# Optimization experiments

Hardware: AMD Instinct MI355X
Metric: run time of the kernel (lower is better)

The kernel has to match this reference:

```python
import jax, jax.numpy as jnp
import numpy as np

D_MODEL = 1024
N_HEAD = 16
D_K = 64
D_V = 64
D_INNER = 4096
MAX_REL = 16
EPS = 1e-6


def _rel_index(length_q, length_k):
    # Shaw-style clipped relative distance matrix -> indices into embedding table
    dist = jnp.arange(length_k)[None, :] - jnp.arange(length_q)[:, None]
    return jnp.clip(dist, -MAX_REL, MAX_REL) + MAX_REL  # [Lq, Lk] in [0, 2*MAX_REL]


def _layer_norm(x, gamma, beta):
    mu = jnp.mean(x, axis=-1, keepdims=True)
    var = jnp.var(x, axis=-1, keepdims=True)
    return (x - mu) / jnp.sqrt(var + EPS) * gamma + beta


def setup_inputs() -> dict:
    key = jax.random.key(0)
    ks = jax.random.split(key, 16)
    B, L = 8, 1024
    s = 0.02
    inp = {
        "q": jax.random.normal(ks[0], (B, L, D_MODEL), jnp.float32),
        "k": jax.random.normal(ks[1], (B, L, D_MODEL), jnp.float32),
        "v": jax.random.normal(ks[2], (B, L, D_MODEL), jnp.float32),
        "wq": jax.random.normal(ks[3], (D_MODEL, D_MODEL), jnp.float32) * s,
        "bq": jnp.zeros((D_MODEL,), jnp.float32),
        "wk": jax.random.normal(ks[4], (D_MODEL, D_MODEL), jnp.float32) * s,
        "bk": jnp.zeros((D_MODEL,), jnp.float32),
        "wv": jax.random.normal(ks[5], (D_MODEL, D_MODEL), jnp.float32) * s,
        "bv": jnp.zeros((D_MODEL,), jnp.float32),
        "wfc": jax.random.normal(ks[6], (D_MODEL, D_MODEL), jnp.float32) * s,
        "bfc": jnp.zeros((D_MODEL,), jnp.float32),
        "w1": jax.random.normal(ks[7], (D_MODEL, D_INNER), jnp.float32) * s,
        "b1": jnp.zeros((D_INNER,), jnp.float32),
        "w2": jax.random.normal(ks[8], (D_INNER, D_MODEL), jnp.float32) * s,
        "b2": jnp.zeros((D_MODEL,), jnp.float32),
        "ln_g": jnp.ones((D_MODEL,), jnp.float32),
        "ln_b": jnp.zeros((D_MODEL,), jnp.float32),
        "rel_k": jax.random.normal(ks[9], (2 * MAX_REL + 1, D_K), jnp.float32) * s,
        "rel_v": jax.random.normal(ks[10], (2 * MAX_REL + 1, D_V), jnp.float32) * s,
    }
    return inp


def reference(q, k, v, wq, bq, wk, bk, wv, bv, wfc, bfc, w1, b1, w2, b2, ln_g, ln_b, rel_k, rel_v):
    B, Lq, _ = q.shape
    Lk = k.shape[1]
    residual = q

    Q = q @ wq + bq  # [B, Lq, D]
    K = k @ wk + bk
    V = v @ wv + bv

    Qh = Q.reshape(B, Lq, N_HEAD, D_K)  # [B, Lq, H, dk]
    Kh = K.reshape(B, Lk, N_HEAD, D_K)
    Vh = V.reshape(B, Lk, N_HEAD, D_V)

    # content-content scores
    attn1 = jnp.einsum("bqhd,bkhd->bhqk", Qh, Kh)
    # content-position scores (Shaw relative position)
    idx = _rel_index(Lq, Lk)  # [Lq, Lk]
    k2 = rel_k[idx]           # [Lq, Lk, dk]
    attn2 = jnp.einsum("bqhd,qkd->bhqk", Qh, k2)

    attn = (attn1 + attn2) / jnp.sqrt(jnp.float32(D_K))
    attn = jax.nn.softmax(attn, axis=-1)  # dropout = identity (eval)

    weight1 = jnp.einsum("bhqk,bkhd->bhqd", attn, Vh)
    v2 = rel_v[idx]  # [Lq, Lk, dv]
    weight2 = jnp.einsum("bhqk,qkd->bhqd", attn, v2)

    out = (weight1 + weight2).transpose(0, 2, 1, 3).reshape(B, Lq, N_HEAD * D_V)
    out = out @ wfc + bfc
    out = out + residual
    out = _layer_norm(out, ln_g, ln_b)

    residual = out
    out2 = jax.nn.relu(out @ w1 + b1) @ w2 + b2
    out = _layer_norm(out2 + residual, ln_g, ln_b)  # same LN params reused, as in source
    return out
```

## Files before the change

### kernel.cpp

```cpp
#include <hip/hip_runtime.h>
#include <stdint.h>


typedef __bf16 bf16x8 __attribute__((ext_vector_type(8)));
typedef float  f32x4  __attribute__((ext_vector_type(4)));

__device__ __forceinline__ unsigned short f2bf(float f) {
  __bf16 h = (__bf16)f;
  union { __bf16 h; unsigned short u; } x; x.h = h;
  return x.u;
}
__device__ __forceinline__ float bf2f(unsigned short h) {
  union { unsigned u; float f; } x; x.u = ((unsigned)h) << 16; return x.f;
}

__device__ __forceinline__ void gload_lds16(
    const unsigned short* g,
    __attribute__((address_space(3))) unsigned int* l) {
  __builtin_amdgcn_global_load_lds(
      (const __attribute__((address_space(1))) unsigned int*)g, l, 16, 0, 0);
}

template<int EPI>
__global__ __launch_bounds__(256, 4) void gemm_bt(
    const unsigned short* __restrict__ A,
    const unsigned short* __restrict__ Bt,
    const float* __restrict__ bias0,
    const float* __restrict__ bias1,
    const float* __restrict__ bias2,
    void* __restrict__ Cout,
    int M, int N, int K,
    size_t sA, size_t sB, size_t sC)
{
  __shared__ __align__(16) unsigned short As[2][128 * 32];
  __shared__ __align__(16) unsigned short Bs[2][128 * 32];
  const int tid = threadIdx.x;
  const int lane = tid & 63, wv = tid >> 6;
  const int lq = lane >> 4, lm = lane & 15;
  const int wr = wv >> 1, wc = wv & 1;

  const int z = blockIdx.z;
  const float* bias = (z == 0) ? bias0 : (z == 1) ? bias1 : bias2;
  A  += (size_t)z * sA;
  Bt += (size_t)z * sB;

  const int nx = gridDim.x;
  const int nwg = nx * gridDim.y;
  int bid = blockIdx.y * nx + blockIdx.x;
  bid = (bid & 7) * (nwg >> 3) + (bid >> 3);
  const int m0 = (bid / nx) * 128, n0 = (bid % nx) * 128;

  const unsigned short* ga0 = A  + (size_t)(m0 + (tid >> 2)) * K + (tid & 3) * 8;
  const unsigned short* gb0 = Bt + (size_t)(n0 + (tid >> 2)) * K + (tid & 3) * 8;
  const size_t rstep = (size_t)64 * K;

  __attribute__((address_space(3))) unsigned int* lA =
      (__attribute__((address_space(3))) unsigned int*)As + wv * 256;
  __attribute__((address_space(3))) unsigned int* lB =
      (__attribute__((address_space(3))) unsigned int*)Bs + wv * 256;

  const char* fa = (const char*)As + (wr * 64 + lm) * 64 + lq * 16;
  const char* fb = (const char*)Bs + (wc * 64 + lm) * 64 + lq * 16;

  f32x4 acc[4][4] = {};

  auto compute_tile = [&](int b) {
    bf16x8 af[4], bfr[4];
    #pragma unroll
    for (int i = 0; i < 4; ++i) af[i]  = *(const bf16x8*)(fa + b * 8192 + i * 1024);
    #pragma unroll
    for (int j = 0; j < 4; ++j) bfr[j] = *(const bf16x8*)(fb + b * 8192 + j * 1024);
    #pragma unroll
    for (int i = 0; i < 4; ++i)
      #pragma unroll
      for (int j = 0; j < 4; ++j)
        acc[i][j] = __builtin_amdgcn_mfma_f32_16x16x32_bf16(af[i], bfr[j], acc[i][j], 0, 0, 0);
  };

  const int nk = K >> 5;
  gload_lds16(ga0,         lA);
  gload_lds16(ga0 + rstep, lA + 1024);
  gload_lds16(gb0,         lB);
  gload_lds16(gb0 + rstep, lB + 1024);
  ga0 += 32; gb0 += 32;
  __syncthreads();

  int cur = 0;
  for (int kt = 0; kt < nk - 1; ++kt) {
    const int nb = cur ^ 1;
    gload_lds16(ga0,         lA + nb * 2048);
    gload_lds16(ga0 + rstep, lA + nb * 2048 + 1024);
    gload_lds16(gb0,         lB + nb * 2048);
    gload_lds16(gb0 + rstep, lB + nb * 2048 + 1024);
    ga0 += 32; gb0 += 32;
    compute_tile(cur);
    __syncthreads();
    cur = nb;
  }
  compute_tile(cur);

  #pragma unroll
  for (int i = 0; i < 4; ++i) {
    #pragma unroll
    for (int j = 0; j < 4; ++j) {
      const int col = n0 + wc * 64 + j * 16 + lm;
      const float bv = bias[col];
      #pragma unroll
      for (int r = 0; r < 4; ++r) {
        const int row = m0 + wr * 64 + i * 16 + lq * 4 + r;
        float v = acc[i][j][r] + bv;
        if (EPI == 2) v = fmaxf(v, 0.0f);
        if (EPI == 1) ((float*)Cout)[(size_t)row * N + col] = v;
        else ((unsigned short*)Cout + (size_t)z * sC)[(size_t)row * N + col] = f2bf(v);
      }
    }
  }
}

__global__ __launch_bounds__(256) void tcast(
    const float* __restrict__ in, unsigned short* __restrict__ out, int R, int C)
{
  __shared__ float tile[32][33];
  const int tx = threadIdx.x & 31, ty = threadIdx.x >> 5;
  const int r0 = blockIdx.y * 32, c0 = blockIdx.x * 32;
  #pragma unroll
  for (int s = 0; s < 4; ++s)
    tile[ty + s * 8][tx] = in[(size_t)(r0 + ty + s * 8) * C + c0 + tx];
  __syncthreads();
  #pragma unroll
  for (int s = 0; s < 4; ++s)
    out[(size_t)(c0 + ty + s * 8) * R + r0 + tx] = f2bf(tile[tx][ty + s * 8]);
}

__global__ __launch_bounds__(256) void cast4(
    const float* __restrict__ in, unsigned short* __restrict__ out, int n)
{
  int i = (blockIdx.x * 256 + threadIdx.x) * 4;
  if (i < n) {
    float4 v = *(const float4*)(in + i);
    ushort4 o;
    o.x = f2bf(v.x); o.y = f2bf(v.y); o.z = f2bf(v.z); o.w = f2bf(v.w);
    *(ushort4*)(out + i) = o;
  }
}

__global__ __launch_bounds__(256) void vtrans(
    const unsigned short* __restrict__ VP, unsigned short* __restrict__ VPT)
{
  __shared__ unsigned short tile[64 * 66];
  const int pt = blockIdx.x, h = blockIdx.y, b = blockIdx.z;
  const int tid = threadIdx.x;
  const int p = tid >> 2, c0 = (tid & 3) * 16;
  const unsigned short* src = VP + (size_t)(b * 1024 + pt * 64 + p) * 1024 + h * 64 + c0;
  union { uint4 q; unsigned int u[4]; } t0, t1;
  t0.q = *(const uint4*)src;
  t1.q = *(const uint4*)(src + 8);
  #pragma unroll
  for (int e = 0; e < 4; ++e) {
    *(unsigned int*)&tile[p * 66 + c0 + e * 2]     = t0.u[e];
    *(unsigned int*)&tile[p * 66 + c0 + 8 + e * 2] = t1.u[e];
  }
  __syncthreads();
  const int d = tid >> 2, p0 = (tid & 3) * 16;
  union { uint4 q[2]; unsigned short s[16]; } ob;
  #pragma unroll
  for (int e = 0; e < 16; ++e) ob.s[e] = tile[(p0 + e) * 66 + d];
  unsigned short* dst = VPT + ((size_t)(h * 64 + d) * 8 + b) * 1024 + pt * 64 + p0;
  *(uint4*)dst       = ob.q[0];
  *(uint4*)(dst + 8) = ob.q[1];
}

__global__ __launch_bounds__(256, 3) void attn_flash(
    const unsigned short* __restrict__ Qp,
    const unsigned short* __restrict__ Kp,
    const unsigned short* __restrict__ VPT,
    const float* __restrict__ relk,
    const float* __restrict__ relv,
    unsigned short* __restrict__ ctx)
{
  int id = (blockIdx.z * gridDim.y + blockIdx.y) * gridDim.x + blockIdx.x;
  id = (id & 7) * 256 + (id >> 3);
  const int qt = id & 15, h = (id >> 4) & 15, b = id >> 8;

  const int tid = threadIdx.x;
  const int lane = tid & 63, wv = tid >> 6;
  const int lq = lane >> 4, lm = lane & 15;

  __shared__ __align__(16) unsigned short Kt[64][72];
  __shared__ __align__(16) unsigned short Vt[64][72];
  __shared__ __align__(16) unsigned short Pt[64][72];
  __shared__ __align__(16) unsigned short relvT[64][32];
  __shared__ float qrel_s[64][33];
  __shared__ float Racc[64][33];

  const float CE = 0.125f * 1.44269504088896340736f;

  const int tok0 = b * 1024 + qt * 64;

  for (int i = tid; i < 64 * 33; i += 256) {
    const int rr = i / 33, ss = i - rr * 33;
    Racc[rr][ss] = 0.0f;
  }
  for (int i = tid; i < 64 * 32; i += 256) {
    const int dd = i >> 5, ss = i & 31;
    relvT[dd][ss] = f2bf(relv[ss * 64 + dd]);
  }

  bf16x8 qf0, qf1;
  {
    const unsigned short* qg = Qp + (size_t)(tok0 + wv * 16 + lm) * 1024 + h * 64;
    qf0 = *(const bf16x8*)(qg + lq * 8);
    qf1 = *(const bf16x8*)(qg + 32 + lq * 8);
  }

  #pragma unroll
  for (int t = 0; t < 3; ++t) {
    const int bin = t * 16 + lm;
    union { bf16x8 v; unsigned short s[8]; } rk0, rk1;
    #pragma unroll
    for (int e = 0; e < 8; ++e) { rk0.s[e] = 0; rk1.s[e] = 0; }
    if (bin < 33) {
      const float* rp = relk + bin * 64 + lq * 8;
      #pragma unroll
      for (int e = 0; e < 8; ++e) {
        rk0.s[e] = f2bf(rp[e]);
        rk1.s[e] = f2bf(rp[32 + e]);
      }
    }
    f32x4 Sr = {};
    Sr = __builtin_amdgcn_mfma_f32_16x16x32_bf16(qf0, rk0.v, Sr, 0, 0, 0);
    Sr = __builtin_amdgcn_mfma_f32_16x16x32_bf16(qf1, rk1.v, Sr, 0, 0, 0);
    if (bin < 33) {
      #pragma unroll
      for (int r = 0; r < 4; ++r) qrel_s[wv * 16 + lq * 4 + r][bin] = Sr[r] * CE;
    }
  }
  __syncthreads();

  float q0a[4], q32a[4];
  #pragma unroll
  for (int r = 0; r < 4; ++r) {
    const int rowl = wv * 16 + lq * 4 + r;
    q0a[r]  = qrel_s[rowl][0];
    q32a[r] = qrel_s[rowl][32];
  }

  union { bf16x8 v; unsigned short s[8]; } one8;
  #pragma unroll
  for (int e = 0; e < 8; ++e) one8.s[e] = 0x3F80;

  f32x4 Oa[4] = {};
  f32x4 Rs = {};
  float r0a[4] = {0, 0, 0, 0}, r32a[4] = {0, 0, 0, 0};

  const int srow = tid >> 2, scol = (tid & 3) * 16;
  const unsigned short* kg = Kp + (size_t)(b * 1024 + srow) * 1024 + h * 64 + scol;
  const unsigned short* vg = VPT + ((size_t)(h * 64 + srow) * 8 + b) * 1024 + scol;
  const int qa0 = qt * 64 + wv * 16;

  const int pread = wv * 16 + ((lm & 3) << 2) + (lm >> 2);

  uint4 rk0_ = *(const uint4*)(kg);
  uint4 rk1_ = *(const uint4*)(kg + 8);
  uint4 rv0_ = *(const uint4*)(vg);
  uint4 rv1_ = *(const uint4*)(vg + 8);

  for (int kt = 0; kt < 16; ++kt) {
    __syncthreads();
    *(uint4*)&Kt[srow][scol]     = rk0_;
    *(uint4*)&Kt[srow][scol + 8] = rk1_;
    *(uint4*)&Vt[srow][scol]     = rv0_;
    *(uint4*)&Vt[srow][scol + 8] = rv1_;
    if (kt < 15) {
      kg += 64 * 1024;
      vg += 64;
      rk0_ = *(const uint4*)(kg);
      rk1_ = *(const uint4*)(kg + 8);
      rv0_ = *(const uint4*)(vg);
      rv1_ = *(const uint4*)(vg + 8);
    }
    __syncthreads();

    #pragma unroll
    for (int tj = 0; tj < 4; ++tj) {
      bf16x8 kf0 = *(const bf16x8*)(&Kt[tj * 16 + lm][lq * 8]);
      bf16x8 kf1 = *(const bf16x8*)(&Kt[tj * 16 + lm][32 + lq * 8]);
      f32x4 S = {};
      S = __builtin_amdgcn_mfma_f32_16x16x32_bf16(qf0, kf0, S, 0, 0, 0);
      S = __builtin_amdgcn_mfma_f32_16x16x32_bf16(qf1, kf1, S, 0, 0, 0);
      const int c0 = kt * 64 + tj * 16;
      const int prow0 = wv * 16 + lq;
      if (c0 + 31 <= qa0) {
        #pragma unroll
        for (int r = 0; r < 4; ++r) {
          const float p = __builtin_amdgcn_exp2f(fmaf(S[r], CE, q0a[r]));
          r0a[r] += p;
          Pt[prow0 + r * 4][tj * 16 + lm] = f2bf(p);
        }
      } else if (c0 >= qa0 + 31) {
        #pragma unroll
        for (int r = 0; r < 4; ++r) {
          const float p = __builtin_amdgcn_exp2f(fmaf(S[r], CE, q32a[r]));
          r32a[r] += p;
          Pt[prow0 + r * 4][tj * 16 + lm] = f2bf(p);
        }
      } else {
        const int kpos = c0 + lm;
        #pragma unroll
        for (int r = 0; r < 4; ++r) {
          const int rowl = wv * 16 + lq * 4 + r;
          const int dist = kpos - (qt * 64 + rowl);
          const int bin = (dist < -16 ? 0 : (dist > 16 ? 32 : dist + 16));
          const float p = __builtin_amdgcn_exp2f(fmaf(S[r], CE, qrel_s[rowl][bin]));
          if (bin == 0)       r0a[r]  += p;
          else if (bin == 32) r32a[r] += p;
          else Racc[rowl][bin] = p;
          Pt[prow0 + r * 4][tj * 16 + lm] = f2bf(p);
        }
      }
    }
    __syncthreads();
    bf16x8 pf0 = *(const bf16x8*)(&Pt[pread][lq * 8]);
    bf16x8 pf1 = *(const bf16x8*)(&Pt[pread][32 + lq * 8]);
    Rs = __builtin_amdgcn_mfma_f32_16x16x32_bf16(pf0, one8.v, Rs, 0, 0, 0);
    Rs = __builtin_amdgcn_mfma_f32_16x16x32_bf16(pf1, one8.v, Rs, 0, 0, 0);
    #pragma unroll
    for (int dt = 0; dt < 4; ++dt) {
      bf16x8 vf0 = *(const bf16x8*)(&Vt[dt * 16 + lm][lq * 8]);
      bf16x8 vf1 = *(const bf16x8*)(&Vt[dt * 16 + lm][32 + lq * 8]);
      Oa[dt] = __builtin_amdgcn_mfma_f32_16x16x32_bf16(pf0, vf0, Oa[dt], 0, 0, 0);
      Oa[dt] = __builtin_amdgcn_mfma_f32_16x16x32_bf16(pf1, vf1, Oa[dt], 0, 0, 0);
    }
  }

  #pragma unroll
  for (int r = 0; r < 4; ++r) {
    #pragma unroll
    for (int off = 1; off < 16; off <<= 1) {
      r0a[r]  += __shfl_xor(r0a[r],  off, 64);
      r32a[r] += __shfl_xor(r32a[r], off, 64);
    }
  }
  if (lm == 0) {
    #pragma unroll
    for (int r = 0; r < 4; ++r) Racc[wv * 16 + lq * 4 + r][0] = r0a[r];
  }
  __syncthreads();
  for (int i = tid; i < 64 * 32; i += 256) {
    const int rr = i >> 5, cc = i & 31;
    Pt[rr][cc] = f2bf(Racc[rr][cc]);
  }
  __syncthreads();

  bf16x8 raf = *(const bf16x8*)(&Pt[wv * 16 + lm][lq * 8]);
  #pragma unroll
  for (int dt = 0; dt < 4; ++dt) {
    bf16x8 rvb = *(const bf16x8*)(&relvT[dt * 16 + lm][lq * 8]);
    f32x4 O2 = {};
    O2 = __builtin_amdgcn_mfma_f32_16x16x32_bf16(raf, rvb, O2, 0, 0, 0);
    const float rv32 = relv[32 * 64 + dt * 16 + lm];
    #pragma unroll
    for (int r = 0; r < 4; ++r) {
      const int rowl = wv * 16 + lq * 4 + r;
      const float v = (Oa[dt][r] + O2[r] + r32a[r] * rv32) / Rs[r];
      ctx[(size_t)(tok0 + rowl) * 1024 + h * 64 + dt * 16 + lm] = f2bf(v);
    }
  }
}

template<bool WB>
__global__ __launch_bounds__(256) void ln_res(
    const float* __restrict__ x, const float* __restrict__ res,
    const float* __restrict__ g, const float* __restrict__ bta,
    float* __restrict__ of, unsigned short* __restrict__ ob)
{
  const int row = blockIdx.x;
  const int tid = threadIdx.x;
  __shared__ float red[8];
  const size_t base = (size_t)row * 1024 + tid * 4;
  const float4 xv = *(const float4*)(x + base);
  const float4 rv = *(const float4*)(res + base);
  float v0 = xv.x + rv.x, v1 = xv.y + rv.y, v2 = xv.z + rv.z, v3 = xv.w + rv.w;
  float s1 = v0 + v1 + v2 + v3;
  float s2 = v0 * v0 + v1 * v1 + v2 * v2 + v3 * v3;
  #pragma unroll
  for (int off = 1; off < 64; off <<= 1) {
    s1 += __shfl_xor(s1, off, 64);
    s2 += __shfl_xor(s2, off, 64);
  }
  const int wv = tid >> 6;
  if ((tid & 63) == 0) { red[wv * 2] = s1; red[wv * 2 + 1] = s2; }
  __syncthreads();
  s1 = red[0] + red[2] + red[4] + red[6];
  s2 = red[1] + red[3] + red[5] + red[7];
  const float mean = s1 * (1.f / 1024.f);
  const float var = s2 * (1.f / 1024.f) - mean * mean;
  const float rstd = rsqrtf(var + 1e-6f);
  const float4 gv = *(const float4*)(g + tid * 4);
  const float4 bv = *(const float4*)(bta + tid * 4);
  float y0 = (v0 - mean) * rstd * gv.x + bv.x;
  float y1 = (v1 - mean) * rstd * gv.y + bv.y;
  float y2 = (v2 - mean) * rstd * gv.z + bv.z;
  float y3 = (v3 - mean) * rstd * gv.w + bv.w;
  float4 yo; yo.x = y0; yo.y = y1; yo.z = y2; yo.w = y3;
  *(float4*)(of + base) = yo;
  if (WB) {
    ushort4 o;
    o.x = f2bf(y0); o.y = f2bf(y1); o.z = f2bf(y2); o.w = f2bf(y3);
    *(ushort4*)(ob + base) = o;
  }
}

extern "C" void kernel_launch(void* const* d_in, const int* in_sizes, int n_in,
                              void* d_out, int out_size, void* d_ws, size_t ws_size,
                              hipStream_t stream) {
  (void)in_sizes; (void)n_in; (void)out_size; (void)ws_size;
  const float* q    = (const float*)d_in[0];
  const float* k    = (const float*)d_in[1];
  const float* v    = (const float*)d_in[2];
  const float* wq   = (const float*)d_in[3];
  const float* bq   = (const float*)d_in[4];
  const float* wk   = (const float*)d_in[5];
  const float* bk   = (const float*)d_in[6];
  const float* wv_  = (const float*)d_in[7];
  const float* bv   = (const float*)d_in[8];
  const float* wfc  = (const float*)d_in[9];
  const float* bfc  = (const float*)d_in[10];
  const float* w1   = (const float*)d_in[11];
  const float* b1   = (const float*)d_in[12];
  const float* w2   = (const float*)d_in[13];
  const float* b2   = (const float*)d_in[14];
  const float* ln_g = (const float*)d_in[15];
  const float* ln_b = (const float*)d_in[16];
  const float* rel_k = (const float*)d_in[17];
  const float* rel_v = (const float*)d_in[18];

  char* ws = (char*)d_ws;
  const size_t MB = 1ull << 20;
  unsigned short* WQT  = (unsigned short*)(ws + 0 * MB);
  unsigned short* WKT  = (unsigned short*)(ws + 2 * MB);
  unsigned short* WVT  = (unsigned short*)(ws + 4 * MB);
  unsigned short* WFCT = (unsigned short*)(ws + 6 * MB);
  unsigned short* W1T  = (unsigned short*)(ws + 8 * MB);
  unsigned short* W2T  = (unsigned short*)(ws + 16 * MB);
  unsigned short* QP   = (unsigned short*)(ws + 24 * MB);
  unsigned short* KP   = (unsigned short*)(ws + 40 * MB);
  unsigned short* VP   = (unsigned short*)(ws + 56 * MB);
  unsigned short* QBF  = (unsigned short*)(ws + 72 * MB);
  unsigned short* KBF  = (unsigned short*)(ws + 88 * MB);
  unsigned short* VBF  = (unsigned short*)(ws + 104 * MB);
  unsigned short* VPT  = QBF;
  unsigned short* CTX  = KBF;
  float*          OTMP = (float*)(ws + 104 * MB);
  float*          X1F  = (float*)(ws + 24 * MB);
  unsigned short* X1BF = VP;
  unsigned short* HBUF = (unsigned short*)(ws + 72 * MB);
  float*          Y2   = (float*)(ws + 136 * MB);

  const dim3 blk(256);
  const int NTOK = 8192;

  tcast<<<dim3(32, 32), blk, 0, stream>>>(wq, WQT, 1024, 1024);
  tcast<<<dim3(32, 32), blk, 0, stream>>>(wk, WKT, 1024, 1024);
  tcast<<<dim3(32, 32), blk, 0, stream>>>(wv_, WVT, 1024, 1024);
  tcast<<<dim3(32, 32), blk, 0, stream>>>(wfc, WFCT, 1024, 1024);
  tcast<<<dim3(128, 32), blk, 0, stream>>>(w1, W1T, 1024, 4096);
  tcast<<<dim3(32, 128), blk, 0, stream>>>(w2, W2T, 4096, 1024);
  cast4<<<8192, blk, 0, stream>>>(q, QBF, NTOK * 1024);
  cast4<<<8192, blk, 0, stream>>>(k, KBF, NTOK * 1024);
  cast4<<<8192, blk, 0, stream>>>(v, VBF, NTOK * 1024);

  gemm_bt<0><<<dim3(8, 64, 3), blk, 0, stream>>>(
      QBF, WQT, bq, bk, bv, QP, NTOK, 1024, 1024,
      (size_t)8 * MB, (size_t)1 * MB, (size_t)8 * MB);

  vtrans<<<dim3(16, 16, 8), blk, 0, stream>>>(VP, VPT);

  attn_flash<<<dim3(16, 16, 8), blk, 0, stream>>>(QP, KP, VPT, rel_k, rel_v, CTX);

  gemm_bt<1><<<dim3(8, 64), blk, 0, stream>>>(CTX, WFCT, bfc, bfc, bfc, OTMP,
                                              NTOK, 1024, 1024, 0, 0, 0);
  ln_res<true><<<8192, blk, 0, stream>>>(OTMP, q, ln_g, ln_b, X1F, X1BF);
  gemm_bt<2><<<dim3(32, 64), blk, 0, stream>>>(X1BF, W1T, b1, b1, b1, HBUF,
                                               NTOK, 4096, 1024, 0, 0, 0);
  gemm_bt<1><<<dim3(8, 64), blk, 0, stream>>>(HBUF, W2T, b2, b2, b2, Y2,
                                              NTOK, 1024, 4096, 0, 0, 0);
  ln_res<false><<<8192, blk, 0, stream>>>(Y2, X1F, ln_g, ln_b, (float*)d_out, nullptr);
}
```

Baseline: 610.9 us.

## Triple-buffer GEMM LDS pipeline and load attention K/V fragments directly from global

The GEMM moves from double to triple buffering with async global-to-LDS loads, explicit vmcnt waits and a single barrier per k-step, so loads stay two tiles ahead of compute. The attention kernel drops the K/V shared-memory staging and its barriers and reads MFMA fragments straight from global memory (L2/L1), with occupancy raised to 4. The attention change removes the P-tile barrier before Pt is read, and each wave only reads its own 16 rows of Pt, so that should still be safe. Direct global fragment loads may cost more latency and bandwidth than LDS reuse across the 4 waves, and the larger GEMM LDS footprint lowers its occupancy hint.

```diff
diff --git a/kernel.cpp b/kernel.cpp
--- a/kernel.cpp
+++ b/kernel.cpp
@@ -22,7 +22,7 @@
 }
 
 template<int EPI>
-__global__ __launch_bounds__(256, 4) void gemm_bt(
+__global__ __launch_bounds__(256, 3) void gemm_bt(
     const unsigned short* __restrict__ A,
     const unsigned short* __restrict__ Bt,
     const float* __restrict__ bias0,
@@ -32,8 +32,8 @@
     int M, int N, int K,
     size_t sA, size_t sB, size_t sC)
 {
-  __shared__ __align__(16) unsigned short As[2][128 * 32];
-  __shared__ __align__(16) unsigned short Bs[2][128 * 32];
+  __shared__ __align__(16) unsigned short As[3][128 * 32];
+  __shared__ __align__(16) unsigned short Bs[3][128 * 32];
   const int tid = threadIdx.x;
   const int lane = tid & 63, wv = tid >> 6;
   const int lq = lane >> 4, lm = lane & 15;
@@ -64,12 +64,19 @@
 
   f32x4 acc[4][4] = {};
 
-  auto compute_tile = [&](int b) {
+  auto stage = [&](int buf) {
+    gload_lds16(ga0,         lA + buf * 2048);
+    gload_lds16(ga0 + rstep, lA + buf * 2048 + 1024);
+    gload_lds16(gb0,         lB + buf * 2048);
+    gload_lds16(gb0 + rstep, lB + buf * 2048 + 1024);
+    ga0 += 32; gb0 += 32;
+  };
+  auto compute_tile = [&](int buf) {
     bf16x8 af[4], bfr[4];
     #pragma unroll
-    for (int i = 0; i < 4; ++i) af[i]  = *(const bf16x8*)(fa + b * 8192 + i * 1024);
-    #pragma unroll
-    for (int j = 0; j < 4; ++j) bfr[j] = *(const bf16x8*)(fb + b * 8192 + j * 1024);
+    for (int i = 0; i < 4; ++i) af[i]  = *(const bf16x8*)(fa + buf * 8192 + i * 1024);
+    #pragma unroll
+    for (int j = 0; j < 4; ++j) bfr[j] = *(const bf16x8*)(fb + buf * 8192 + j * 1024);
     #pragma unroll
     for (int i = 0; i < 4; ++i)
       #pragma unroll
@@ -78,26 +85,25 @@
   };
 
   const int nk = K >> 5;
-  gload_lds16(ga0,         lA);
-  gload_lds16(ga0 + rstep, lA + 1024);
-  gload_lds16(gb0,         lB);
-  gload_lds16(gb0 + rstep, lB + 1024);
-  ga0 += 32; gb0 += 32;
-  __syncthreads();
-
-  int cur = 0;
-  for (int kt = 0; kt < nk - 1; ++kt) {
-    const int nb = cur ^ 1;
-    gload_lds16(ga0,         lA + nb * 2048);
-    gload_lds16(ga0 + rstep, lA + nb * 2048 + 1024);
-    gload_lds16(gb0,         lB + nb * 2048);
-    gload_lds16(gb0 + rstep, lB + nb * 2048 + 1024);
-    ga0 += 32; gb0 += 32;
-    compute_tile(cur);
-    __syncthreads();
-    cur = nb;
-  }
-  compute_tile(cur);
+  stage(0);
+  stage(1);
+  int t = 0;
+  for (; t < nk - 2; ++t) {
+    asm volatile("s_waitcnt vmcnt(4)" ::: "memory");
+    __builtin_amdgcn_s_barrier();
+    __builtin_amdgcn_sched_barrier(0);
+    stage((t + 2) % 3);
+    compute_tile(t % 3);
+  }
+  asm volatile("s_waitcnt vmcnt(4)" ::: "memory");
+  __builtin_amdgcn_s_barrier();
+  __builtin_amdgcn_sched_barrier(0);
+  compute_tile(t % 3);
+  ++t;
+  asm volatile("s_waitcnt vmcnt(0)" ::: "memory");
+  __builtin_amdgcn_s_barrier();
+  __builtin_amdgcn_sched_barrier(0);
+  compute_tile(t % 3);
 
   #pragma unroll
   for (int i = 0; i < 4; ++i) {
@@ -170,7 +176,7 @@
   *(uint4*)(dst + 8) = ob.q[1];
 }
 
-__global__ __launch_bounds__(256, 3) void attn_flash(
+__global__ __launch_bounds__(256, 4) void attn_flash(
     const unsigned short* __restrict__ Qp,
     const unsigned short* __restrict__ Kp,
     const unsigned short* __restrict__ VPT,
@@ -186,8 +192,6 @@
   const int lane = tid & 63, wv = tid >> 6;
   const int lq = lane >> 4, lm = lane & 15;
 
-  __shared__ __align__(16) unsigned short Kt[64][72];
-  __shared__ __align__(16) unsigned short Vt[64][72];
   __shared__ __align__(16) unsigned short Pt[64][72];
   __shared__ __align__(16) unsigned short relvT[64][32];
   __shared__ float qrel_s[64][33];
@@ -253,38 +257,21 @@
   f32x4 Rs = {};
   float r0a[4] = {0, 0, 0, 0}, r32a[4] = {0, 0, 0, 0};
 
-  const int srow = tid >> 2, scol = (tid & 3) * 16;
-  const unsigned short* kg = Kp + (size_t)(b * 1024 + srow) * 1024 + h * 64 + scol;
-  const unsigned short* vg = VPT + ((size_t)(h * 64 + srow) * 8 + b) * 1024 + scol;
   const int qa0 = qt * 64 + wv * 16;
 
   const int pread = wv * 16 + ((lm & 3) << 2) + (lm >> 2);
 
-  uint4 rk0_ = *(const uint4*)(kg);
-  uint4 rk1_ = *(const uint4*)(kg + 8);
-  uint4 rv0_ = *(const uint4*)(vg);
-  uint4 rv1_ = *(const uint4*)(vg + 8);
+  const unsigned short* kbase = Kp + (size_t)(b * 1024) * 1024 + h * 64;
+  const unsigned short* vbase = VPT + ((size_t)(h * 64) * 8 + b) * 1024;
 
   for (int kt = 0; kt < 16; ++kt) {
-    __syncthreads();
-    *(uint4*)&Kt[srow][scol]     = rk0_;
-    *(uint4*)&Kt[srow][scol + 8] = rk1_;
-    *(uint4*)&Vt[srow][scol]     = rv0_;
-    *(uint4*)&Vt[srow][scol + 8] = rv1_;
-    if (kt < 15) {
-      kg += 64 * 1024;
-      vg += 64;
-      rk0_ = *(const uint4*)(kg);
-      rk1_ = *(const uint4*)(kg + 8);
-      rv0_ = *(const uint4*)(vg);
-      rv1_ = *(const uint4*)(vg + 8);
-    }
-    __syncthreads();
+    const unsigned short* kp = kbase + (size_t)(kt * 64) * 1024;
 
     #pragma unroll
     for (int tj = 0; tj < 4; ++tj) {
-      bf16x8 kf0 = *(const bf16x8*)(&Kt[tj * 16 + lm][lq * 8]);
-      bf16x8 kf1 = *(const bf16x8*)(&Kt[tj * 16 + lm][32 + lq * 8]);
+      const unsigned short* krow = kp + (size_t)(tj * 16 + lm) * 1024 + lq * 8;
+      bf16x8 kf0 = *(const bf16x8*)(krow);
+      bf16x8 kf1 = *(const bf16x8*)(krow + 32);
       f32x4 S = {};
       S = __builtin_amdgcn_mfma_f32_16x16x32_bf16(qf0, kf0, S, 0, 0, 0);
       S = __builtin_amdgcn_mfma_f32_16x16x32_bf16(qf1, kf1, S, 0, 0, 0);
@@ -319,15 +306,15 @@
         }
       }
     }
-    __syncthreads();
     bf16x8 pf0 = *(const bf16x8*)(&Pt[pread][lq * 8]);
     bf16x8 pf1 = *(const bf16x8*)(&Pt[pread][32 + lq * 8]);
     Rs = __builtin_amdgcn_mfma_f32_16x16x32_bf16(pf0, one8.v, Rs, 0, 0, 0);
     Rs = __builtin_amdgcn_mfma_f32_16x16x32_bf16(pf1, one8.v, Rs, 0, 0, 0);
     #pragma unroll
     for (int dt = 0; dt < 4; ++dt) {
-      bf16x8 vf0 = *(const bf16x8*)(&Vt[dt * 16 + lm][lq * 8]);
-      bf16x8 vf1 = *(const bf16x8*)(&Vt[dt * 16 + lm][32 + lq * 8]);
+      const unsigned short* vrow = vbase + (size_t)(dt * 16 + lm) * 8192 + kt * 64 + lq * 8;
+      bf16x8 vf0 = *(const bf16x8*)(vrow);
+      bf16x8 vf1 = *(const bf16x8*)(vrow + 32);
       Oa[dt] = __builtin_amdgcn_mfma_f32_16x16x32_bf16(pf0, vf0, Oa[dt], 0, 0, 0);
       Oa[dt] = __builtin_amdgcn_mfma_f32_16x16x32_bf16(pf1, vf1, Oa[dt], 0, 0, 0);
     }
```

Result: slower. 763.4 us (+25.0%).

## Rewrite GEMM as 256x128 tile, 8-wave, triple-buffered K=64 pipeline

Applied to the files above, without the earlier changes.

The bf16 GEMM kernel now uses 512-thread blocks computing 256x128 output tiles with K-steps of 64. It stages operands into a three-buffer LDS ring with global_load_lds, waits on explicit vmcnt counts, and interleaves barriers and setprio around the MFMA groups so loads overlap compute. The aim is more data reuse per LDS load and better latency hiding than the old double-buffered 128x128, K=32 loop. Separately, a __syncthreads is removed in the attention kernel between writing P to LDS and reading it back, which could introduce a race between waves. Larger LDS use (144 KB) and more registers per block reduce occupancy.

```diff
diff --git a/kernel.cpp b/kernel.cpp
--- a/kernel.cpp
+++ b/kernel.cpp
@@ -9,9 +9,6 @@
   __bf16 h = (__bf16)f;
   union { __bf16 h; unsigned short u; } x; x.h = h;
   return x.u;
-}
-__device__ __forceinline__ float bf2f(unsigned short h) {
-  union { unsigned u; float f; } x; x.u = ((unsigned)h) << 16; return x.f;
 }
 
 __device__ __forceinline__ void gload_lds16(
@@ -22,7 +19,7 @@
 }
 
 template<int EPI>
-__global__ __launch_bounds__(256, 4) void gemm_bt(
+__global__ __launch_bounds__(512, 2) void gemm_bt(
     const unsigned short* __restrict__ A,
     const unsigned short* __restrict__ Bt,
     const float* __restrict__ bias0,
@@ -32,12 +29,11 @@
     int M, int N, int K,
     size_t sA, size_t sB, size_t sC)
 {
-  __shared__ __align__(16) unsigned short As[2][128 * 32];
-  __shared__ __align__(16) unsigned short Bs[2][128 * 32];
+  __shared__ __align__(16) unsigned short S[3 * 24576];
   const int tid = threadIdx.x;
   const int lane = tid & 63, wv = tid >> 6;
   const int lq = lane >> 4, lm = lane & 15;
-  const int wr = wv >> 1, wc = wv & 1;
+  const int wr = wv >> 2, wc = wv & 3;
 
   const int z = blockIdx.z;
   const float* bias = (z == 0) ? bias0 : (z == 1) ? bias1 : bias2;
@@ -48,66 +44,84 @@
   const int nwg = nx * gridDim.y;
   int bid = blockIdx.y * nx + blockIdx.x;
   bid = (bid & 7) * (nwg >> 3) + (bid >> 3);
-  const int m0 = (bid / nx) * 128, n0 = (bid % nx) * 128;
-
-  const unsigned short* ga0 = A  + (size_t)(m0 + (tid >> 2)) * K + (tid & 3) * 8;
-  const unsigned short* gb0 = Bt + (size_t)(n0 + (tid >> 2)) * K + (tid & 3) * 8;
-  const size_t rstep = (size_t)64 * K;
-
-  __attribute__((address_space(3))) unsigned int* lA =
-      (__attribute__((address_space(3))) unsigned int*)As + wv * 256;
-  __attribute__((address_space(3))) unsigned int* lB =
-      (__attribute__((address_space(3))) unsigned int*)Bs + wv * 256;
-
-  const char* fa = (const char*)As + (wr * 64 + lm) * 64 + lq * 16;
-  const char* fb = (const char*)Bs + (wc * 64 + lm) * 64 + lq * 16;
-
-  f32x4 acc[4][4] = {};
-
-  auto compute_tile = [&](int b) {
-    bf16x8 af[4], bfr[4];
-    #pragma unroll
-    for (int i = 0; i < 4; ++i) af[i]  = *(const bf16x8*)(fa + b * 8192 + i * 1024);
-    #pragma unroll
-    for (int j = 0; j < 4; ++j) bfr[j] = *(const bf16x8*)(fb + b * 8192 + j * 1024);
-    #pragma unroll
-    for (int i = 0; i < 4; ++i)
+  const int m0 = (bid / nx) * 256, n0 = (bid % nx) * 128;
+
+  const unsigned short* ga = A  + (size_t)(m0 + (tid >> 3)) * K + (tid & 7) * 8;
+  const unsigned short* gb = Bt + (size_t)(n0 + (tid >> 3)) * K + (tid & 7) * 8;
+
+  __attribute__((address_space(3))) unsigned int* lbase =
+      (__attribute__((address_space(3))) unsigned int*)S;
+
+  f32x4 acc[8][2] = {};
+
+  auto stage = [&](int buf) {
+    __attribute__((address_space(3))) unsigned int* lA = lbase + buf * 12288 + wv * 256;
+    __attribute__((address_space(3))) unsigned int* lB = lA + 8192;
+    #pragma unroll
+    for (int g = 0; g < 4; ++g)
+      gload_lds16(ga + (size_t)(g * 64) * K, lA + g * 2048);
+    #pragma unroll
+    for (int g = 0; g < 2; ++g)
+      gload_lds16(gb + (size_t)(g * 64) * K, lB + g * 2048);
+    ga += 64; gb += 64;
+  };
+
+  const char* fa = (const char*)S + (wr * 128 + lm) * 128 + lq * 16;
+  const char* fb = (const char*)S + 32768 + (wc * 32 + lm) * 128 + lq * 16;
+
+  auto compute_tile = [&](int buf) {
+    const char* ba = fa + buf * 49152;
+    const char* bb = fb + buf * 49152;
+    bf16x8 bfr[2][2];
+    #pragma unroll
+    for (int j = 0; j < 2; ++j)
       #pragma unroll
-      for (int j = 0; j < 4; ++j)
-        acc[i][j] = __builtin_amdgcn_mfma_f32_16x16x32_bf16(af[i], bfr[j], acc[i][j], 0, 0, 0);
+      for (int kk = 0; kk < 2; ++kk)
+        bfr[j][kk] = *(const bf16x8*)(bb + j * 2048 + kk * 64);
+    #pragma unroll
+    for (int q = 0; q < 4; ++q) {
+      bf16x8 af[2][2];
+      #pragma unroll
+      for (int ii = 0; ii < 2; ++ii)
+        #pragma unroll
+        for (int kk = 0; kk < 2; ++kk)
+          af[ii][kk] = *(const bf16x8*)(ba + (q * 2 + ii) * 2048 + kk * 64);
+      __builtin_amdgcn_s_barrier();
+      __builtin_amdgcn_s_setprio(1);
+      #pragma unroll
+      for (int ii = 0; ii < 2; ++ii)
+        #pragma unroll
+        for (int j = 0; j < 2; ++j)
+          #pragma unroll
+          for (int kk = 0; kk < 2; ++kk)
+            acc[q * 2 + ii][j] = __builtin_amdgcn_mfma_f32_16x16x32_bf16(
+                af[ii][kk], bfr[j][kk], acc[q * 2 + ii][j], 0, 0, 0);
+      __builtin_amdgcn_s_setprio(0);
+      __builtin_amdgcn_s_barrier();
+    }
   };
 
-  const int nk = K >> 5;
-  gload_lds16(ga0,         lA);
-  gload_lds16(ga0 + rstep, lA + 1024);
-  gload_lds16(gb0,         lB);
-  gload_lds16(gb0 + rstep, lB + 1024);
-  ga0 += 32; gb0 += 32;
-  __syncthreads();
-
-  int cur = 0;
-  for (int kt = 0; kt < nk - 1; ++kt) {
-    const int nb = cur ^ 1;
-    gload_lds16(ga0,         lA + nb * 2048);
-    gload_lds16(ga0 + rstep, lA + nb * 2048 + 1024);
-    gload_lds16(gb0,         lB + nb * 2048);
-    gload_lds16(gb0 + rstep, lB + nb * 2048 + 1024);
-    ga0 += 32; gb0 += 32;
-    compute_tile(cur);
-    __syncthreads();
-    cur = nb;
-  }
-  compute_tile(cur);
-
-  #pragma unroll
-  for (int i = 0; i < 4; ++i) {
-    #pragma unroll
-    for (int j = 0; j < 4; ++j) {
-      const int col = n0 + wc * 64 + j * 16 + lm;
+  const int nt = K >> 6;
+  stage(0);
+  stage(1);
+  for (int t = 0; t < nt; ++t) {
+    if (t + 1 < nt) asm volatile("s_waitcnt vmcnt(6)" ::: "memory");
+    else            asm volatile("s_waitcnt vmcnt(0)" ::: "memory");
+    __builtin_amdgcn_s_barrier();
+    __builtin_amdgcn_sched_barrier(0);
+    if (t + 2 < nt) stage((t + 2) % 3);
+    compute_tile(t % 3);
+  }
+
+  #pragma unroll
+  for (int i = 0; i < 8; ++i) {
+    #pragma unroll
+    for (int j = 0; j < 2; ++j) {
+      const int col = n0 + wc * 32 + j * 16 + lm;
       const float bv = bias[col];
       #pragma unroll
       for (int r = 0; r < 4; ++r) {
-        const int row = m0 + wr * 64 + i * 16 + lq * 4 + r;
+        const int row = m0 + wr * 128 + i * 16 + lq * 4 + r;
         float v = acc[i][j][r] + bv;
         if (EPI == 2) v = fmaxf(v, 0.0f);
         if (EPI == 1) ((float*)Cout)[(size_t)row * N + col] = v;
@@ -319,7 +333,6 @@
         }
       }
     }
-    __syncthreads();
     bf16x8 pf0 = *(const bf16x8*)(&Pt[pread][lq * 8]);
     bf16x8 pf1 = *(const bf16x8*)(&Pt[pread][32 + lq * 8]);
     Rs = __builtin_amdgcn_mfma_f32_16x16x32_bf16(pf0, one8.v, Rs, 0, 0, 0);
@@ -458,6 +471,7 @@
   float*          Y2   = (float*)(ws + 136 * MB);
 
   const dim3 blk(256);
+  const dim3 gblk(512);
   const int NTOK = 8192;
 
   tcast<<<dim3(32, 32), blk, 0, stream>>>(wq, WQT, 1024, 1024);
@@ -470,7 +484,7 @@
   cast4<<<8192, blk, 0, stream>>>(k, KBF, NTOK * 1024);
   cast4<<<8192, blk, 0, stream>>>(v, VBF, NTOK * 1024);
 
-  gemm_bt<0><<<dim3(8, 64, 3), blk, 0, stream>>>(
+  gemm_bt<0><<<dim3(8, 32, 3), gblk, 0, stream>>>(
       QBF, WQT, bq, bk, bv, QP, NTOK, 1024, 1024,
       (size_t)8 * MB, (size_t)1 * MB, (size_t)8 * MB);
 
@@ -478,12 +492,12 @@
 
   attn_flash<<<dim3(16, 16, 8), blk, 0, stream>>>(QP, KP, VPT, rel_k, rel_v, CTX);
 
-  gemm_bt<1><<<dim3(8, 64), blk, 0, stream>>>(CTX, WFCT, bfc, bfc, bfc, OTMP,
-                                              NTOK, 1024, 1024, 0, 0, 0);
+  gemm_bt<1><<<dim3(8, 32), gblk, 0, stream>>>(CTX, WFCT, bfc, bfc, bfc, OTMP,
+                                               NTOK, 1024, 1024, 0, 0, 0);
   ln_res<true><<<8192, blk, 0, stream>>>(OTMP, q, ln_g, ln_b, X1F, X1BF);
-  gemm_bt<2><<<dim3(32, 64), blk, 0, stream>>>(X1BF, W1T, b1, b1, b1, HBUF,
-                                               NTOK, 4096, 1024, 0, 0, 0);
-  gemm_bt<1><<<dim3(8, 64), blk, 0, stream>>>(HBUF, W2T, b2, b2, b2, Y2,
-                                              NTOK, 1024, 4096, 0, 0, 0);
+  gemm_bt<2><<<dim3(32, 32), gblk, 0, stream>>>(X1BF, W1T, b1, b1, b1, HBUF,
+                                                NTOK, 4096, 1024, 0, 0, 0);
+  gemm_bt<1><<<dim3(8, 32), gblk, 0, stream>>>(HBUF, W2T, b2, b2, b2, Y2,
+                                               NTOK, 1024, 4096, 0, 0, 0);
   ln_res<false><<<8192, blk, 0, stream>>>(Y2, X1F, ln_g, ln_b, (float*)d_out, nullptr);
 }
```

Result: slower. 713.3 us (+16.7%).
